# Kernel optimization log

Measured on AMD Instinct MI355X. Metric: run time of the kernel, lower is better.

The kernel has to match this reference:

```python
import jax, jax.numpy as jnp
import numpy as np

N, D, HID, ATT, B, NC = 131072, 1024, 256, 128, 64, 2
EPS = 1e-5

def _ln(h, g, b):
    mu = jnp.mean(h, axis=-1, keepdims=True)
    var = jnp.mean((h - mu) ** 2, axis=-1, keepdims=True)
    return (h - mu) * jax.lax.rsqrt(var + EPS) * g + b

def _gelu(x):
    return jax.nn.gelu(x, approximate=False)  # torch nn.GELU default (erf)

def setup_inputs() -> dict:
    key = jax.random.key(0)
    ks = jax.random.split(key, 16)
    def w(k, shape, fan_in):
        return (jax.random.normal(k, shape, jnp.float32) / np.sqrt(fan_in)).astype(jnp.float32)
    # sorted, every bag non-empty (~equal sizes)
    segment_ids = ((jnp.arange(N) * B) // N).astype(jnp.int32)
    return {
        "x": jax.random.normal(ks[0], (N, D), jnp.float32),
        "segment_ids": segment_ids,
        "W1": w(ks[1], (D, HID), D), "b1": jnp.zeros((HID,), jnp.float32),
        "g1": jnp.ones((HID,), jnp.float32), "be1": jnp.zeros((HID,), jnp.float32),
        "W2": w(ks[2], (HID, HID), HID), "b2": jnp.zeros((HID,), jnp.float32),
        "g2": jnp.ones((HID,), jnp.float32), "be2": jnp.zeros((HID,), jnp.float32),
        "Wv": w(ks[3], (HID, ATT), HID), "bv": jnp.zeros((ATT,), jnp.float32),
        "Wu": w(ks[4], (HID, ATT), HID), "bu": jnp.zeros((ATT,), jnp.float32),
        "Ww": w(ks[5], (ATT, 1), ATT), "bw": jnp.zeros((1,), jnp.float32),
        "Wc1": w(ks[6], (HID, HID // 2), HID), "bc1": jnp.zeros((HID // 2,), jnp.float32),
        "Wc2": w(ks[7], (HID // 2, NC), HID // 2), "bc2": jnp.zeros((NC,), jnp.float32),
    }

def reference(x, segment_ids, W1, b1, g1, be1, W2, b2, g2, be2,
              Wv, bv, Wu, bu, Ww, bw, Wc1, bc1, Wc2, bc2):
    # encoder (dropout = identity at inference)
    h = _gelu(_ln(x @ W1 + b1, g1, be1))          # [N, HID]
    h = _gelu(_ln(h @ W2 + b2, g2, be2))          # [N, HID]
    # gated attention logits
    a = (jnp.tanh(h @ Wv + bv) * jax.nn.sigmoid(h @ Wu + bu)) @ Ww + bw  # [N, 1]
    a = a[:, 0]                                    # [N]
    # per-bag (segment) softmax
    m = jax.ops.segment_max(a, segment_ids, num_segments=B)             # [B]
    e = jnp.exp(a - m[segment_ids])
    s = jax.ops.segment_sum(e, segment_ids, num_segments=B)             # [B]
    attn = e / s[segment_ids]                                           # [N]
    # attention-weighted bag pooling
    z = jax.ops.segment_sum(attn[:, None] * h, segment_ids, num_segments=B)  # [B, HID]
    # classifier
    logits = _gelu(z @ Wc1 + bc1) @ Wc2 + bc2       # [B, NC]
    return logits
```

## Files before the change

kernel.cpp:

```cpp
#include <hip/hip_runtime.h>
#include <math.h>

#define N_TOK  131072
#define DIM    1024
#define HIDN   256
#define ATTN   128
#define NSEG   64
#define SEGLEN 2048
#define NCLS   2
#define EPSLN  1e-5f

typedef __attribute__((ext_vector_type(8))) short  short8;
typedef __attribute__((ext_vector_type(4))) float  f32x4;

__device__ __forceinline__ unsigned short f2bf(float f) {
    unsigned int u = __float_as_uint(f);
    u += 0x7fffu + ((u >> 16) & 1u);
    return (unsigned short)(u >> 16);
}
__device__ __forceinline__ float bf2f(unsigned short h) {
    return __uint_as_float(((unsigned int)h) << 16);
}
__device__ __forceinline__ float gelu_exact(float x) {
    return 0.5f * x * (1.0f + erff(x * 0.70710678118654752f));
}

__global__ __launch_bounds__(256) void prep_weights(const float* __restrict__ W1,
                                                    const float* __restrict__ W2,
                                                    const float* __restrict__ Wv,
                                                    const float* __restrict__ Wu,
                                                    const float* __restrict__ bv,
                                                    const float* __restrict__ bu,
                                                    unsigned short* __restrict__ W1f,
                                                    unsigned short* __restrict__ W2f,
                                                    unsigned short* __restrict__ Wvuf,
                                                    float* __restrict__ bvu) {
    const int b = blockIdx.x, tid = threadIdx.x;
    if (b == 192) {
        bvu[tid] = (tid < 128) ? bv[tid] : bu[tid - 128];
        return;
    }
    const int lane = tid & 63;
    const int lr = lane & 15, lq = lane >> 4;
    short8 sv;
    if (b < 128) {
        const int idx = b * 256 + tid;
        const int rem = idx >> 6;
        const int j = rem & 3, t = (rem >> 2) & 31, w = rem >> 7;
        const int n = 64 * w + 16 * j + lr;
        const int k = t * 32 + lq * 8;
#pragma unroll
        for (int e = 0; e < 8; e++) sv[e] = (short)f2bf(W1[(size_t)(k + e) * HIDN + n]);
        *(short8*)&W1f[(size_t)idx * 8] = sv;
    } else if (b < 160) {
        const int idx = (b - 128) * 256 + tid;
        const int rem = idx >> 6;
        const int j = rem & 3, t = (rem >> 2) & 7, w = rem >> 5;
        const int n = 64 * w + 16 * j + lr;
        const int k = t * 32 + lq * 8;
#pragma unroll
        for (int e = 0; e < 8; e++) sv[e] = (short)f2bf(W2[(size_t)(k + e) * HIDN + n]);
        *(short8*)&W2f[(size_t)idx * 8] = sv;
    } else {
        const int idx = (b - 160) * 256 + tid;
        const int rem = idx >> 6;
        const int j = rem & 3, t = (rem >> 2) & 7, w = rem >> 5;
        const int n = 64 * w + 16 * j + lr;
        const int k = t * 32 + lq * 8;
#pragma unroll
        for (int e = 0; e < 8; e++) {
            const float v = (n < 128) ? Wv[(size_t)(k + e) * ATTN + n]
                                      : Wu[(size_t)(k + e) * ATTN + (n - 128)];
            sv[e] = (short)f2bf(v);
        }
        *(short8*)&Wvuf[(size_t)idx * 8] = sv;
    }
}

__global__ __launch_bounds__(256, 4) void fused_mlp_score(
    const float* __restrict__ x,
    const unsigned short* __restrict__ W1f,
    const unsigned short* __restrict__ W2f,
    const unsigned short* __restrict__ Wvuf,
    const float* __restrict__ b1, const float* __restrict__ g1, const float* __restrict__ be1,
    const float* __restrict__ b2, const float* __restrict__ g2, const float* __restrict__ be2,
    const float* __restrict__ bvu, const float* __restrict__ Ww, const float* __restrict__ bw,
    unsigned short* __restrict__ h2b, float* __restrict__ scores) {
    __shared__ __align__(16) char smem[35840];
    auto As  = (unsigned short (*)[40])smem;
    auto HT  = (unsigned short (*)[264])smem;
    auto red = (float (*)[4][64])(smem + 33792);

    const int tid  = threadIdx.x;
    const int wave = tid >> 6, lane = tid & 63;
    const int lr = lane & 15, lq = lane >> 4;
    const int srow = tid >> 2, skq = (tid & 3) * 8;
    const size_t row0 = (size_t)blockIdx.x * 64;

    f32x4 acc[4][4];
    auto zero_acc = [&]() {
#pragma unroll
        for (int i = 0; i < 4; i++)
#pragma unroll
            for (int j = 0; j < 4; j++) acc[i][j] = (f32x4)0.0f;
    };

    auto ln_epilogue = [&](const float* bias, const float* gamma, const float* beta, bool toGlobal) {
        float bjv[4];
#pragma unroll
        for (int j = 0; j < 4; j++) bjv[j] = bias[wave * 64 + 16 * j + lr];
#pragma unroll
        for (int i = 0; i < 4; i++)
#pragma unroll
            for (int j = 0; j < 4; j++)
#pragma unroll
                for (int r = 0; r < 4; r++) acc[i][j][r] += bjv[j];
#pragma unroll
        for (int i = 0; i < 4; i++)
#pragma unroll
            for (int r = 0; r < 4; r++) {
                float s = 0.0f, sq = 0.0f;
#pragma unroll
                for (int j = 0; j < 4; j++) { float v = acc[i][j][r]; s += v; sq += v * v; }
#pragma unroll
                for (int m = 1; m < 16; m <<= 1) { s += __shfl_xor(s, m); sq += __shfl_xor(sq, m); }
                if (lr == 0) {
                    red[0][wave][16 * i + 4 * lq + r] = s;
                    red[1][wave][16 * i + 4 * lq + r] = sq;
                }
            }
        __syncthreads();
        float gj[4], bej[4];
#pragma unroll
        for (int j = 0; j < 4; j++) {
            gj[j]  = gamma[wave * 64 + 16 * j + lr];
            bej[j] = beta[wave * 64 + 16 * j + lr];
        }
#pragma unroll
        for (int i = 0; i < 4; i++)
#pragma unroll
            for (int r = 0; r < 4; r++) {
                const int row = 16 * i + 4 * lq + r;
                const float s  = red[0][0][row] + red[0][1][row] + red[0][2][row] + red[0][3][row];
                const float sq = red[1][0][row] + red[1][1][row] + red[1][2][row] + red[1][3][row];
                const float mu  = s * (1.0f / HIDN);
                const float var = sq * (1.0f / HIDN) - mu * mu;
                const float rs  = rsqrtf(var + EPSLN);
#pragma unroll
                for (int j = 0; j < 4; j++) {
                    const int col = wave * 64 + 16 * j + lr;
                    const unsigned short hv = f2bf(gelu_exact((acc[i][j][r] - mu) * rs * gj[j] + bej[j]));
                    HT[row][col] = hv;
                    if (toGlobal) h2b[(row0 + row) * 256 + col] = hv;
                }
            }
        __syncthreads();
    };

    auto loadX = [&](int t, short8& aw) {
        const float* p = &x[(row0 + srow) * DIM + t * 32 + skq];
        float4 v0 = *(const float4*)p;
        float4 v1 = *(const float4*)(p + 4);
        aw[0] = (short)f2bf(v0.x); aw[1] = (short)f2bf(v0.y);
        aw[2] = (short)f2bf(v0.z); aw[3] = (short)f2bf(v0.w);
        aw[4] = (short)f2bf(v1.x); aw[5] = (short)f2bf(v1.y);
        aw[6] = (short)f2bf(v1.z); aw[7] = (short)f2bf(v1.w);
    };

    zero_acc();
    {
        short8 xw;
        loadX(0, xw);
        *(short8*)&As[0 * 64 + srow][skq] = xw;
        __syncthreads();
        const short8* wbase = (const short8*)W1f + (size_t)wave * 32 * 4 * 64 + lane;
        for (int t = 0; t < 32; ++t) {
            const bool more = (t + 1 < 32);
            if (more) loadX(t + 1, xw);
            const short8* wp = wbase + (size_t)t * 256;
            short8 b[4], a[4];
#pragma unroll
            for (int j = 0; j < 4; j++) b[j] = wp[j * 64];
#pragma unroll
            for (int i = 0; i < 4; i++) a[i] = *(const short8*)&As[(t & 1) * 64 + 16 * i + lr][lq * 8];
#pragma unroll
            for (int i = 0; i < 4; i++)
#pragma unroll
                for (int j = 0; j < 4; j++)
                    acc[i][j] = __builtin_amdgcn_mfma_f32_16x16x32_bf16(a[i], b[j], acc[i][j], 0, 0, 0);
            if (more) *(short8*)&As[((t + 1) & 1) * 64 + srow][skq] = xw;
            __syncthreads();
        }
    }
    ln_epilogue(b1, g1, be1, false);

    zero_acc();
    {
        const short8* wbase = (const short8*)W2f + (size_t)wave * 8 * 4 * 64 + lane;
#pragma unroll 2
        for (int t = 0; t < 8; ++t) {
            const short8* wp = wbase + (size_t)t * 256;
            short8 b[4], a[4];
#pragma unroll
            for (int j = 0; j < 4; j++) b[j] = wp[j * 64];
#pragma unroll
            for (int i = 0; i < 4; i++) a[i] = *(const short8*)&HT[16 * i + lr][t * 32 + lq * 8];
#pragma unroll
            for (int i = 0; i < 4; i++)
#pragma unroll
                for (int j = 0; j < 4; j++)
                    acc[i][j] = __builtin_amdgcn_mfma_f32_16x16x32_bf16(a[i], b[j], acc[i][j], 0, 0, 0);
        }
    }
    ln_epilogue(b2, g2, be2, true);

    zero_acc();
    {
        const short8* wbase = (const short8*)Wvuf + (size_t)wave * 8 * 4 * 64 + lane;
#pragma unroll 2
        for (int t = 0; t < 8; ++t) {
            const short8* wp = wbase + (size_t)t * 256;
            short8 b[4], a[4];
#pragma unroll
            for (int j = 0; j < 4; j++) b[j] = wp[j * 64];
#pragma unroll
            for (int i = 0; i < 4; i++) a[i] = *(const short8*)&HT[16 * i + lr][t * 32 + lq * 8];
#pragma unroll
            for (int i = 0; i < 4; i++)
#pragma unroll
                for (int j = 0; j < 4; j++)
                    acc[i][j] = __builtin_amdgcn_mfma_f32_16x16x32_bf16(a[i], b[j], acc[i][j], 0, 0, 0);
        }
    }
    __syncthreads();

    {
        float bjv[4];
#pragma unroll
        for (int j = 0; j < 4; j++) bjv[j] = bvu[wave * 64 + 16 * j + lr];
#pragma unroll
        for (int i = 0; i < 4; i++)
#pragma unroll
            for (int j = 0; j < 4; j++)
#pragma unroll
                for (int r = 0; r < 4; r++) acc[i][j][r] += bjv[j];

        float (*us)[129] = (float (*)[129])smem;
        float (*pw)[64]  = (float (*)[64])(smem + 33792);
        if (wave >= 2) {
            const int cb = (wave - 2) * 64;
#pragma unroll
            for (int i = 0; i < 4; i++)
#pragma unroll
                for (int j = 0; j < 4; j++)
#pragma unroll
                    for (int r = 0; r < 4; r++)
                        us[16 * i + 4 * lq + r][cb + 16 * j + lr] =
                            1.0f / (1.0f + expf(-acc[i][j][r]));
        }
        __syncthreads();
        if (wave < 2) {
            const int cb = wave * 64;
            float wwj[4];
#pragma unroll
            for (int j = 0; j < 4; j++) wwj[j] = Ww[cb + 16 * j + lr];
#pragma unroll
            for (int i = 0; i < 4; i++)
#pragma unroll
                for (int r = 0; r < 4; r++) {
                    const int row = 16 * i + 4 * lq + r;
                    float s = 0.0f;
#pragma unroll
                    for (int j = 0; j < 4; j++)
                        s += tanhf(acc[i][j][r]) * us[row][cb + 16 * j + lr] * wwj[j];
#pragma unroll
                    for (int m = 1; m < 16; m <<= 1) s += __shfl_xor(s, m);
                    if (lr == 0) pw[wave][row] = s;
                }
        }
        __syncthreads();
        if (tid < 64) scores[row0 + tid] = pw[0][tid] + pw[1][tid] + bw[0];
    }
}

__global__ __launch_bounds__(256) void pool_partial(const float* __restrict__ Scores,
                                                    const unsigned short* __restrict__ H,
                                                    float* __restrict__ Zp,
                                                    float* __restrict__ Se) {
    __shared__ float aw[256];
    __shared__ float part[8][256];
    __shared__ float sred[4];
    const int tid = threadIdx.x;
    const size_t rbase = (size_t)blockIdx.x * 256;
    const float e = expf(Scores[rbase + tid]);
    aw[tid] = e;
    float se = e;
#pragma unroll
    for (int o = 32; o > 0; o >>= 1) se += __shfl_down(se, o);
    if ((tid & 63) == 0) sred[tid >> 6] = se;
    __syncthreads();
    const int cg = tid & 31;
    const int rg = tid >> 5;
    float acc[8];
#pragma unroll
    for (int j = 0; j < 8; j++) acc[j] = 0.0f;
    for (int r = rg * 32; r < rg * 32 + 32; ++r) {
        short8 h8 = *(const short8*)&H[(rbase + r) * 256 + cg * 8];
        const float a = aw[r];
#pragma unroll
        for (int j = 0; j < 8; j++) acc[j] += a * bf2f((unsigned short)h8[j]);
    }
#pragma unroll
    for (int j = 0; j < 8; j++) part[rg][cg * 8 + j] = acc[j];
    __syncthreads();
    float s = 0.0f;
#pragma unroll
    for (int gq = 0; gq < 8; gq++) s += part[gq][tid];
    Zp[rbase + tid] = s;
    if (tid == 0) Se[blockIdx.x] = sred[0] + sred[1] + sred[2] + sred[3];
}

__global__ __launch_bounds__(256) void head_kernel(const float* __restrict__ Zp,
                                                   const float* __restrict__ Se,
                                                   const float* __restrict__ Wc1,
                                                   const float* __restrict__ bc1,
                                                   const float* __restrict__ Wc2,
                                                   const float* __restrict__ bc2,
                                                   float* __restrict__ Out) {
    __shared__ float zs[256];
    __shared__ float hs[128];
    __shared__ float red[4];
    const int seg = blockIdx.x, tid = threadIdx.x;
    float z = 0.0f;
#pragma unroll
    for (int c = 0; c < 8; c++) z += Zp[((size_t)seg * 8 + c) * 256 + tid];
    float den = 0.0f;
#pragma unroll
    for (int c = 0; c < 8; c++) den += Se[seg * 8 + c];
    zs[tid] = z / den;
    __syncthreads();
    if (tid < 128) {
        float acc = bc1[tid];
        for (int k = 0; k < 256; k++) acc += zs[k] * Wc1[k * 128 + tid];
        hs[tid] = gelu_exact(acc);
    }
    __syncthreads();
    const int cls = tid >> 7, j = tid & 127;
    float val = hs[j] * Wc2[j * 2 + cls];
#pragma unroll
    for (int o = 32; o > 0; o >>= 1) val += __shfl_down(val, o);
    if ((tid & 63) == 0) red[tid >> 6] = val;
    __syncthreads();
    if (tid < 2) Out[seg * 2 + tid] = red[tid * 2] + red[tid * 2 + 1] + bc2[tid];
}

extern "C" void kernel_launch(void* const* d_in, const int* in_sizes, int n_in,
                              void* d_out, int out_size, void* d_ws, size_t ws_size,
                              hipStream_t stream) {
    const float* x   = (const float*)d_in[0];
    const float* W1  = (const float*)d_in[2];
    const float* b1  = (const float*)d_in[3];
    const float* g1  = (const float*)d_in[4];
    const float* be1 = (const float*)d_in[5];
    const float* W2  = (const float*)d_in[6];
    const float* b2  = (const float*)d_in[7];
    const float* g2  = (const float*)d_in[8];
    const float* be2 = (const float*)d_in[9];
    const float* Wv  = (const float*)d_in[10];
    const float* bv  = (const float*)d_in[11];
    const float* Wu  = (const float*)d_in[12];
    const float* bu  = (const float*)d_in[13];
    const float* Ww  = (const float*)d_in[14];
    const float* bw  = (const float*)d_in[15];
    const float* Wc1 = (const float*)d_in[16];
    const float* bc1 = (const float*)d_in[17];
    const float* Wc2 = (const float*)d_in[18];
    const float* bc2 = (const float*)d_in[19];
    float* out = (float*)d_out;

    char* p = (char*)d_ws;
    unsigned short* h2b    = (unsigned short*)p; p += (size_t)N_TOK * HIDN * 2;
    float*          scores = (float*)p;          p += (size_t)N_TOK * 4;
    unsigned short* W1f    = (unsigned short*)p; p += (size_t)HIDN * DIM * 2;
    unsigned short* W2f    = (unsigned short*)p; p += (size_t)HIDN * HIDN * 2;
    unsigned short* Wvuf   = (unsigned short*)p; p += (size_t)HIDN * HIDN * 2;
    float*          bvu    = (float*)p;          p += 256 * 4;
    float*          Zp     = (float*)p;          p += (size_t)NSEG * 8 * HIDN * 4;
    float*          Se     = (float*)p;          p += (size_t)NSEG * 8 * 4;

    prep_weights<<<193, 256, 0, stream>>>(W1, W2, Wv, Wu, bv, bu, W1f, W2f, Wvuf, bvu);

    fused_mlp_score<<<N_TOK / 64, 256, 0, stream>>>(
        x, W1f, W2f, Wvuf,
        b1, g1, be1, b2, g2, be2,
        bvu, Ww, bw, h2b, scores);

    pool_partial<<<NSEG * 8, 256, 0, stream>>>(scores, h2b, Zp, Se);
    head_kernel<<<NSEG, 256, 0, stream>>>(Zp, Se, Wc1, bc1, Wc2, bc2, out);
}
```

Baseline: 914.2 us.

## Fuse attention pooling into MLP kernel and deepen x/weight prefetch pipeline

Attention pooling moves into the fused MLP kernel. Each 64-row block computes its exp-scores and the weighted sum of h2 directly from shared memory, and writes per-block partials to Zp/Se. This drops the h2b and scores round trips through global memory and removes the pool_partial launch. The Wv/Wu weight layout is interleaved so each wave holds matching tanh and sigmoid columns, which removes the shared-memory sigmoid exchange. The x loads are prefetched three stages ahead, weight fragments are double-buffered, and the occupancy hint drops from 4 to 3 blocks. The risks are higher register pressure and a larger head reduction over 32 partials per segment; the softmax uses no max subtraction, which the code before also did.

```diff
diff --git a/kernel.cpp b/kernel.cpp
--- a/kernel.cpp
+++ b/kernel.cpp
@@ -6,7 +6,7 @@
 #define HIDN   256
 #define ATTN   128
 #define NSEG   64
-#define SEGLEN 2048
+#define NBLK   (N_TOK / 64)
 #define NCLS   2
 #define EPSLN  1e-5f
 
@@ -24,22 +24,23 @@
 __device__ __forceinline__ float gelu_exact(float x) {
     return 0.5f * x * (1.0f + erff(x * 0.70710678118654752f));
 }
+__device__ __forceinline__ short8 cvt8(float4 v0, float4 v1) {
+    short8 r;
+    r[0] = (short)f2bf(v0.x); r[1] = (short)f2bf(v0.y);
+    r[2] = (short)f2bf(v0.z); r[3] = (short)f2bf(v0.w);
+    r[4] = (short)f2bf(v1.x); r[5] = (short)f2bf(v1.y);
+    r[6] = (short)f2bf(v1.z); r[7] = (short)f2bf(v1.w);
+    return r;
+}
 
 __global__ __launch_bounds__(256) void prep_weights(const float* __restrict__ W1,
                                                     const float* __restrict__ W2,
                                                     const float* __restrict__ Wv,
                                                     const float* __restrict__ Wu,
-                                                    const float* __restrict__ bv,
-                                                    const float* __restrict__ bu,
                                                     unsigned short* __restrict__ W1f,
                                                     unsigned short* __restrict__ W2f,
-                                                    unsigned short* __restrict__ Wvuf,
-                                                    float* __restrict__ bvu) {
+                                                    unsigned short* __restrict__ Wvuf) {
     const int b = blockIdx.x, tid = threadIdx.x;
-    if (b == 192) {
-        bvu[tid] = (tid < 128) ? bv[tid] : bu[tid - 128];
-        return;
-    }
     const int lane = tid & 63;
     const int lr = lane & 15, lq = lane >> 4;
     short8 sv;
@@ -65,27 +66,25 @@
         const int idx = (b - 160) * 256 + tid;
         const int rem = idx >> 6;
         const int j = rem & 3, t = (rem >> 2) & 7, w = rem >> 5;
-        const int n = 64 * w + 16 * j + lr;
+        const int col = 32 * w + 16 * (j & 1) + lr;
         const int k = t * 32 + lq * 8;
-#pragma unroll
-        for (int e = 0; e < 8; e++) {
-            const float v = (n < 128) ? Wv[(size_t)(k + e) * ATTN + n]
-                                      : Wu[(size_t)(k + e) * ATTN + (n - 128)];
-            sv[e] = (short)f2bf(v);
-        }
+        const float* src = (j < 2) ? Wv : Wu;
+#pragma unroll
+        for (int e = 0; e < 8; e++) sv[e] = (short)f2bf(src[(size_t)(k + e) * ATTN + col]);
         *(short8*)&Wvuf[(size_t)idx * 8] = sv;
     }
 }
 
-__global__ __launch_bounds__(256, 4) void fused_mlp_score(
+__global__ __launch_bounds__(256, 3) void fused_mlp_score(
     const float* __restrict__ x,
     const unsigned short* __restrict__ W1f,
     const unsigned short* __restrict__ W2f,
     const unsigned short* __restrict__ Wvuf,
     const float* __restrict__ b1, const float* __restrict__ g1, const float* __restrict__ be1,
     const float* __restrict__ b2, const float* __restrict__ g2, const float* __restrict__ be2,
-    const float* __restrict__ bvu, const float* __restrict__ Ww, const float* __restrict__ bw,
-    unsigned short* __restrict__ h2b, float* __restrict__ scores) {
+    const float* __restrict__ bv, const float* __restrict__ bu,
+    const float* __restrict__ Ww, const float* __restrict__ bw,
+    float* __restrict__ Zp, float* __restrict__ Se) {
     __shared__ __align__(16) char smem[35840];
     auto As  = (unsigned short (*)[40])smem;
     auto HT  = (unsigned short (*)[264])smem;
@@ -105,7 +104,7 @@
             for (int j = 0; j < 4; j++) acc[i][j] = (f32x4)0.0f;
     };
 
-    auto ln_epilogue = [&](const float* bias, const float* gamma, const float* beta, bool toGlobal) {
+    auto ln_epilogue = [&](const float* bias, const float* gamma, const float* beta) {
         float bjv[4];
 #pragma unroll
         for (int j = 0; j < 4; j++) bjv[j] = bias[wave * 64 + 16 * j + lr];
@@ -147,177 +146,127 @@
                 const float var = sq * (1.0f / HIDN) - mu * mu;
                 const float rs  = rsqrtf(var + EPSLN);
 #pragma unroll
-                for (int j = 0; j < 4; j++) {
-                    const int col = wave * 64 + 16 * j + lr;
-                    const unsigned short hv = f2bf(gelu_exact((acc[i][j][r] - mu) * rs * gj[j] + bej[j]));
-                    HT[row][col] = hv;
-                    if (toGlobal) h2b[(row0 + row) * 256 + col] = hv;
-                }
-            }
-        __syncthreads();
-    };
-
-    auto loadX = [&](int t, short8& aw) {
-        const float* p = &x[(row0 + srow) * DIM + t * 32 + skq];
-        float4 v0 = *(const float4*)p;
-        float4 v1 = *(const float4*)(p + 4);
-        aw[0] = (short)f2bf(v0.x); aw[1] = (short)f2bf(v0.y);
-        aw[2] = (short)f2bf(v0.z); aw[3] = (short)f2bf(v0.w);
-        aw[4] = (short)f2bf(v1.x); aw[5] = (short)f2bf(v1.y);
-        aw[6] = (short)f2bf(v1.z); aw[7] = (short)f2bf(v1.w);
+                for (int j = 0; j < 4; j++)
+                    HT[row][wave * 64 + 16 * j + lr] =
+                        f2bf(gelu_exact((acc[i][j][r] - mu) * rs * gj[j] + bej[j]));
+            }
+        __syncthreads();
     };
 
     zero_acc();
     {
-        short8 xw;
-        loadX(0, xw);
-        *(short8*)&As[0 * 64 + srow][skq] = xw;
-        __syncthreads();
-        const short8* wbase = (const short8*)W1f + (size_t)wave * 32 * 4 * 64 + lane;
+        const float* xrow = &x[(row0 + srow) * DIM + skq];
+        const short8* wb = (const short8*)W1f + (size_t)wave * (32 * 4 * 64) + lane;
+        float4 x0[3], x1[3];
+        short8 bq[2][4];
+#pragma unroll
+        for (int s = 0; s < 3; ++s) {
+            x0[s] = *(const float4*)(xrow + 32 * s);
+            x1[s] = *(const float4*)(xrow + 32 * s + 4);
+        }
+#pragma unroll
+        for (int j = 0; j < 4; ++j) bq[0][j] = wb[j * 64];
+        *(short8*)&As[srow][skq] = cvt8(x0[0], x1[0]);
+        __syncthreads();
+#pragma unroll
         for (int t = 0; t < 32; ++t) {
-            const bool more = (t + 1 < 32);
-            if (more) loadX(t + 1, xw);
-            const short8* wp = wbase + (size_t)t * 256;
-            short8 b[4], a[4];
-#pragma unroll
-            for (int j = 0; j < 4; j++) b[j] = wp[j * 64];
-#pragma unroll
-            for (int i = 0; i < 4; i++) a[i] = *(const short8*)&As[(t & 1) * 64 + 16 * i + lr][lq * 8];
-#pragma unroll
-            for (int i = 0; i < 4; i++)
-#pragma unroll
-                for (int j = 0; j < 4; j++)
-                    acc[i][j] = __builtin_amdgcn_mfma_f32_16x16x32_bf16(a[i], b[j], acc[i][j], 0, 0, 0);
-            if (more) *(short8*)&As[((t + 1) & 1) * 64 + srow][skq] = xw;
+            if (t + 3 < 32) {
+                x0[(t + 3) % 3] = *(const float4*)(xrow + 32 * (t + 3));
+                x1[(t + 3) % 3] = *(const float4*)(xrow + 32 * (t + 3) + 4);
+            }
+            if (t + 1 < 32) {
+                const short8* wp = wb + (size_t)(t + 1) * 256;
+#pragma unroll
+                for (int j = 0; j < 4; ++j) bq[(t + 1) & 1][j] = wp[j * 64];
+            }
+            short8 a[4];
+#pragma unroll
+            for (int i = 0; i < 4; ++i)
+                a[i] = *(const short8*)&As[(t & 1) * 64 + 16 * i + lr][lq * 8];
+#pragma unroll
+            for (int i = 0; i < 4; ++i)
+#pragma unroll
+                for (int j = 0; j < 4; ++j)
+                    acc[i][j] = __builtin_amdgcn_mfma_f32_16x16x32_bf16(a[i], bq[t & 1][j], acc[i][j], 0, 0, 0);
+            if (t + 1 < 32)
+                *(short8*)&As[((t + 1) & 1) * 64 + srow][skq] = cvt8(x0[(t + 1) % 3], x1[(t + 1) % 3]);
             __syncthreads();
         }
     }
-    ln_epilogue(b1, g1, be1, false);
+    ln_epilogue(b1, g1, be1);
+
+    auto gemm_ht = [&](const short8* wb) {
+        short8 bq[2][4];
+#pragma unroll
+        for (int j = 0; j < 4; ++j) bq[0][j] = wb[j * 64];
+#pragma unroll
+        for (int t = 0; t < 8; ++t) {
+            if (t + 1 < 8) {
+                const short8* wp = wb + (size_t)(t + 1) * 256;
+#pragma unroll
+                for (int j = 0; j < 4; ++j) bq[(t + 1) & 1][j] = wp[j * 64];
+            }
+            short8 a[4];
+#pragma unroll
+            for (int i = 0; i < 4; ++i)
+                a[i] = *(const short8*)&HT[16 * i + lr][t * 32 + lq * 8];
+#pragma unroll
+            for (int i = 0; i < 4; ++i)
+#pragma unroll
+                for (int j = 0; j < 4; ++j)
+                    acc[i][j] = __builtin_amdgcn_mfma_f32_16x16x32_bf16(a[i], bq[t & 1][j], acc[i][j], 0, 0, 0);
+        }
+    };
 
     zero_acc();
+    gemm_ht((const short8*)W2f + (size_t)wave * (8 * 4 * 64) + lane);
+    ln_epilogue(b2, g2, be2);
+
+    zero_acc();
+    gemm_ht((const short8*)Wvuf + (size_t)wave * (8 * 4 * 64) + lane);
+
     {
-        const short8* wbase = (const short8*)W2f + (size_t)wave * 8 * 4 * 64 + lane;
-#pragma unroll 2
-        for (int t = 0; t < 8; ++t) {
-            const short8* wp = wbase + (size_t)t * 256;
-            short8 b[4], a[4];
-#pragma unroll
-            for (int j = 0; j < 4; j++) b[j] = wp[j * 64];
-#pragma unroll
-            for (int i = 0; i < 4; i++) a[i] = *(const short8*)&HT[16 * i + lr][t * 32 + lq * 8];
-#pragma unroll
-            for (int i = 0; i < 4; i++)
-#pragma unroll
-                for (int j = 0; j < 4; j++)
-                    acc[i][j] = __builtin_amdgcn_mfma_f32_16x16x32_bf16(a[i], b[j], acc[i][j], 0, 0, 0);
-        }
+        float bvv[2], buu[2], wwj[2];
+#pragma unroll
+        for (int j = 0; j < 2; ++j) {
+            bvv[j] = bv[32 * wave + 16 * j + lr];
+            buu[j] = bu[32 * wave + 16 * j + lr];
+            wwj[j] = Ww[32 * wave + 16 * j + lr];
+        }
+        float (*pw)[64] = (float (*)[64])(smem + 33792);
+        float* es = (float*)(smem + 33792 + 1024);
+#pragma unroll
+        for (int i = 0; i < 4; ++i)
+#pragma unroll
+            for (int r = 0; r < 4; ++r) {
+                const int row = 16 * i + 4 * lq + r;
+                float s = 0.0f;
+#pragma unroll
+                for (int j = 0; j < 2; ++j) {
+                    const float vv = acc[i][j][r] + bvv[j];
+                    const float uu = acc[i][j + 2][r] + buu[j];
+                    s += tanhf(vv) * (1.0f / (1.0f + expf(-uu))) * wwj[j];
+                }
+#pragma unroll
+                for (int m = 1; m < 16; m <<= 1) s += __shfl_xor(s, m);
+                if (lr == 0) pw[wave][row] = s;
+            }
+        __syncthreads();
+        if (tid < 64) {
+            const float sc = pw[0][tid] + pw[1][tid] + pw[2][tid] + pw[3][tid] + bw[0];
+            const float e = expf(sc);
+            es[tid] = e;
+            float t2 = e;
+#pragma unroll
+            for (int o = 32; o > 0; o >>= 1) t2 += __shfl_down(t2, o);
+            if (tid == 0) Se[blockIdx.x] = t2;
+        }
+        __syncthreads();
+        float pacc = 0.0f;
+#pragma unroll 8
+        for (int row = 0; row < 64; ++row) pacc += es[row] * bf2f(HT[row][tid]);
+        Zp[(size_t)blockIdx.x * 256 + tid] = pacc;
     }
-    ln_epilogue(b2, g2, be2, true);
-
-    zero_acc();
-    {
-        const short8* wbase = (const short8*)Wvuf + (size_t)wave * 8 * 4 * 64 + lane;
-#pragma unroll 2
-        for (int t = 0; t < 8; ++t) {
-            const short8* wp = wbase + (size_t)t * 256;
-            short8 b[4], a[4];
-#pragma unroll
-            for (int j = 0; j < 4; j++) b[j] = wp[j * 64];
-#pragma unroll
-            for (int i = 0; i < 4; i++) a[i] = *(const short8*)&HT[16 * i + lr][t * 32 + lq * 8];
-#pragma unroll
-            for (int i = 0; i < 4; i++)
-#pragma unroll
-                for (int j = 0; j < 4; j++)
-                    acc[i][j] = __builtin_amdgcn_mfma_f32_16x16x32_bf16(a[i], b[j], acc[i][j], 0, 0, 0);
-        }
-    }
-    __syncthreads();
-
-    {
-        float bjv[4];
-#pragma unroll
-        for (int j = 0; j < 4; j++) bjv[j] = bvu[wave * 64 + 16 * j + lr];
-#pragma unroll
-        for (int i = 0; i < 4; i++)
-#pragma unroll
-            for (int j = 0; j < 4; j++)
-#pragma unroll
-                for (int r = 0; r < 4; r++) acc[i][j][r] += bjv[j];
-
-        float (*us)[129] = (float (*)[129])smem;
-        float (*pw)[64]  = (float (*)[64])(smem + 33792);
-        if (wave >= 2) {
-            const int cb = (wave - 2) * 64;
-#pragma unroll
-            for (int i = 0; i < 4; i++)
-#pragma unroll
-                for (int j = 0; j < 4; j++)
-#pragma unroll
-                    for (int r = 0; r < 4; r++)
-                        us[16 * i + 4 * lq + r][cb + 16 * j + lr] =
-                            1.0f / (1.0f + expf(-acc[i][j][r]));
-        }
-        __syncthreads();
-        if (wave < 2) {
-            const int cb = wave * 64;
-            float wwj[4];
-#pragma unroll
-            for (int j = 0; j < 4; j++) wwj[j] = Ww[cb + 16 * j + lr];
-#pragma unroll
-            for (int i = 0; i < 4; i++)
-#pragma unroll
-                for (int r = 0; r < 4; r++) {
-                    const int row = 16 * i + 4 * lq + r;
-                    float s = 0.0f;
-#pragma unroll
-                    for (int j = 0; j < 4; j++)
-                        s += tanhf(acc[i][j][r]) * us[row][cb + 16 * j + lr] * wwj[j];
-#pragma unroll
-                    for (int m = 1; m < 16; m <<= 1) s += __shfl_xor(s, m);
-                    if (lr == 0) pw[wave][row] = s;
-                }
-        }
-        __syncthreads();
-        if (tid < 64) scores[row0 + tid] = pw[0][tid] + pw[1][tid] + bw[0];
-    }
-}
-
-__global__ __launch_bounds__(256) void pool_partial(const float* __restrict__ Scores,
-                                                    const unsigned short* __restrict__ H,
-                                                    float* __restrict__ Zp,
-                                                    float* __restrict__ Se) {
-    __shared__ float aw[256];
-    __shared__ float part[8][256];
-    __shared__ float sred[4];
-    const int tid = threadIdx.x;
-    const size_t rbase = (size_t)blockIdx.x * 256;
-    const float e = expf(Scores[rbase + tid]);
-    aw[tid] = e;
-    float se = e;
-#pragma unroll
-    for (int o = 32; o > 0; o >>= 1) se += __shfl_down(se, o);
-    if ((tid & 63) == 0) sred[tid >> 6] = se;
-    __syncthreads();
-    const int cg = tid & 31;
-    const int rg = tid >> 5;
-    float acc[8];
-#pragma unroll
-    for (int j = 0; j < 8; j++) acc[j] = 0.0f;
-    for (int r = rg * 32; r < rg * 32 + 32; ++r) {
-        short8 h8 = *(const short8*)&H[(rbase + r) * 256 + cg * 8];
-        const float a = aw[r];
-#pragma unroll
-        for (int j = 0; j < 8; j++) acc[j] += a * bf2f((unsigned short)h8[j]);
-    }
-#pragma unroll
-    for (int j = 0; j < 8; j++) part[rg][cg * 8 + j] = acc[j];
-    __syncthreads();
-    float s = 0.0f;
-#pragma unroll
-    for (int gq = 0; gq < 8; gq++) s += part[gq][tid];
-    Zp[rbase + tid] = s;
-    if (tid == 0) Se[blockIdx.x] = sred[0] + sred[1] + sred[2] + sred[3];
 }
 
 __global__ __launch_bounds__(256) void head_kernel(const float* __restrict__ Zp,
@@ -333,10 +282,10 @@
     const int seg = blockIdx.x, tid = threadIdx.x;
     float z = 0.0f;
 #pragma unroll
-    for (int c = 0; c < 8; c++) z += Zp[((size_t)seg * 8 + c) * 256 + tid];
+    for (int c = 0; c < 32; ++c) z += Zp[((size_t)seg * 32 + c) * 256 + tid];
     float den = 0.0f;
 #pragma unroll
-    for (int c = 0; c < 8; c++) den += Se[seg * 8 + c];
+    for (int c = 0; c < 32; ++c) den += Se[seg * 32 + c];
     zs[tid] = z / den;
     __syncthreads();
     if (tid < 128) {
@@ -379,22 +328,18 @@
     float* out = (float*)d_out;
 
     char* p = (char*)d_ws;
-    unsigned short* h2b    = (unsigned short*)p; p += (size_t)N_TOK * HIDN * 2;
-    float*          scores = (float*)p;          p += (size_t)N_TOK * 4;
-    unsigned short* W1f    = (unsigned short*)p; p += (size_t)HIDN * DIM * 2;
-    unsigned short* W2f    = (unsigned short*)p; p += (size_t)HIDN * HIDN * 2;
-    unsigned short* Wvuf   = (unsigned short*)p; p += (size_t)HIDN * HIDN * 2;
-    float*          bvu    = (float*)p;          p += 256 * 4;
-    float*          Zp     = (float*)p;          p += (size_t)NSEG * 8 * HIDN * 4;
-    float*          Se     = (float*)p;          p += (size_t)NSEG * 8 * 4;
-
-    prep_weights<<<193, 256, 0, stream>>>(W1, W2, Wv, Wu, bv, bu, W1f, W2f, Wvuf, bvu);
-
-    fused_mlp_score<<<N_TOK / 64, 256, 0, stream>>>(
+    unsigned short* W1f  = (unsigned short*)p; p += (size_t)HIDN * DIM * 2;
+    unsigned short* W2f  = (unsigned short*)p; p += (size_t)HIDN * HIDN * 2;
+    unsigned short* Wvuf = (unsigned short*)p; p += (size_t)HIDN * HIDN * 2;
+    float*          Zp   = (float*)p;          p += (size_t)NBLK * HIDN * 4;
+    float*          Se   = (float*)p;          p += (size_t)NBLK * 4;
+
+    prep_weights<<<192, 256, 0, stream>>>(W1, W2, Wv, Wu, W1f, W2f, Wvuf);
+
+    fused_mlp_score<<<NBLK, 256, 0, stream>>>(
         x, W1f, W2f, Wvuf,
         b1, g1, be1, b2, g2, be2,
-        bvu, Ww, bw, h2b, scores);
-
-    pool_partial<<<NSEG * 8, 256, 0, stream>>>(scores, h2b, Zp, Se);
+        bv, bu, Ww, bw, Zp, Se);
+
     head_kernel<<<NSEG, 256, 0, stream>>>(Zp, Se, Wc1, bc1, Wc2, bc2, out);
 }
```

After: 890.1 us. -2.6%, faster.
